# Performance work log

Hardware: AMD Instinct MI355X
Metric: run time of the kernel (lower is better)

Reference implementation:

```python
import jax, jax.numpy as jnp
import numpy as np

EPS = 1e-08


def setup_inputs() -> dict:
    key = jax.random.key(0)
    k1, k2, k3 = jax.random.split(key, 3)
    N, IN_DIM, OUT_DIM = 8192, 512, 512
    h = jax.random.normal(k1, (N, IN_DIM), dtype=jnp.float32)
    adj = jax.random.randint(k2, (N, N), 0, 2, dtype=jnp.int32)
    # nn.Linear(in_dim, out_dim, bias=False) weight: [out_dim, in_dim]
    W = jax.random.normal(k3, (OUT_DIM, IN_DIM), dtype=jnp.float32) * (1.0 / np.sqrt(IN_DIM))
    return {"h": h, "adj": adj, "W": W}


def reference(h, adj, W):
    # Wh = h @ W^T  -> [N, out_dim]
    Wh = h @ W.T
    N = Wh.shape[0]
    norms = jnp.linalg.norm(Wh, axis=1, keepdims=True)  # [N, 1]
    # cosine similarity [N, N]
    sim = (Wh @ Wh.T) / (norms * norms.T + EPS)
    mask = (adj > 0) | jnp.eye(N, dtype=bool)
    sim_masked = jnp.where(mask, sim, -jnp.inf)
    alpha = jax.nn.softmax(sim_masked, axis=1)
    return alpha @ Wh
```

## Files before the change

kernel.cpp:

```cpp
#include <hip/hip_runtime.h>
#include <hip/hip_bf16.h>
#include <stdint.h>

#define NN 8192
#define DD 512

typedef unsigned short u16;
typedef unsigned long long u64;
typedef __attribute__((ext_vector_type(8))) short short8;
typedef __attribute__((ext_vector_type(4))) float f32x4;

__device__ __forceinline__ void gld_lds16(const void* g, void* l) {
  __builtin_amdgcn_global_load_lds(
      (const __attribute__((address_space(1))) uint32_t*)(uintptr_t)g,
      (__attribute__((address_space(3))) uint32_t*)(uintptr_t)l,
      16, 0, 0);
}

__device__ __forceinline__ u16 f2bf(float f) {
  __hip_bfloat16 b = __float2bfloat16(f);
  return __builtin_bit_cast(u16, b);
}

__global__ void fill_kernel(float* __restrict__ p, int n, float v) {
  int i = blockIdx.x * 256 + threadIdx.x;
  int stride = gridDim.x * 256;
  for (; i < n; i += stride) p[i] = v;
}

__global__ void cvt4_kernel(const float4* __restrict__ src, ushort4* __restrict__ dst, int n4) {
  int i = blockIdx.x * 256 + threadIdx.x;
  int stride = gridDim.x * 256;
  for (; i < n4; i += stride) {
    float4 v = src[i];
    ushort4 o;
    o.x = f2bf(v.x); o.y = f2bf(v.y); o.z = f2bf(v.z); o.w = f2bf(v.w);
    dst[i] = o;
  }
}

__global__ void pack_adj_kernel(const int* __restrict__ adj, u16* __restrict__ mask) {
  const int row = blockIdx.x;
  const int t = threadIdx.x;
  const uint4* arow = (const uint4*)(adj + (size_t)row * NN);
  #pragma unroll
  for (int iter = 0; iter < 2; iter++) {
    const int c16 = iter * 256 + t;
    unsigned int bits = 0;
    #pragma unroll
    for (int g = 0; g < 4; g++) {
      uint4 v = arow[c16 * 4 + g];
      bits |= (v.x ? 1u : 0u) << (g * 4 + 0);
      bits |= (v.y ? 1u : 0u) << (g * 4 + 1);
      bits |= (v.z ? 1u : 0u) << (g * 4 + 2);
      bits |= (v.w ? 1u : 0u) << (g * 4 + 3);
    }
    mask[(size_t)row * (NN / 16) + c16] = (u16)bits;
  }
}

__global__ void rownorm_kernel(const float* __restrict__ Wh, float* __restrict__ invn) {
  int row = blockIdx.x;
  int l = threadIdx.x;
  const float4* p = (const float4*)(Wh + (size_t)row * DD);
  float4 a = p[l], b = p[l + 64];
  float s = a.x*a.x + a.y*a.y + a.z*a.z + a.w*a.w
          + b.x*b.x + b.y*b.y + b.z*b.z + b.w*b.w;
  #pragma unroll
  for (int off = 32; off; off >>= 1) s += __shfl_down(s, off);
  if (l == 0) invn[row] = 1.0f / sqrtf(s);
}

__global__ void u_wht_kernel(const float* __restrict__ Wh, const float* __restrict__ invn,
                             u16* __restrict__ U, u16* __restrict__ WhT) {
  __shared__ float tile[64][65];
  int i0 = blockIdx.x * 64, d0 = blockIdx.y * 64;
  int c = threadIdx.x & 63, rb = threadIdx.x >> 6;
  #pragma unroll
  for (int r = rb; r < 64; r += 4) {
    float v = Wh[(size_t)(i0 + r) * DD + d0 + c];
    tile[r][c] = v;
    U[(size_t)(i0 + r) * DD + d0 + c] = f2bf(v * invn[i0 + r]);
  }
  __syncthreads();
  #pragma unroll
  for (int r = rb; r < 64; r += 4) {
    WhT[(size_t)(d0 + r) * NN + i0 + c] = f2bf(tile[c][r]);
  }
}

__global__ void reduce_scale_kernel(float4* __restrict__ out, const float4* __restrict__ part1,
                                    const float* __restrict__ den) {
  int i4 = blockIdx.x * 256 + threadIdx.x;
  const int row = i4 >> 7;
  const float dinv = 1.0f / den[row];
  float4 a = out[i4], b = part1[i4];
  a.x = (a.x + b.x) * dinv;
  a.y = (a.y + b.y) * dinv;
  a.z = (a.z + b.z) * dinv;
  a.w = (a.w + b.w) * dinv;
  out[i4] = a;
}

template <int MODE>
__global__ void __launch_bounds__(256) gemm_bt(
    const u16* __restrict__ A, const u16* __restrict__ B,
    int Nn, int K, int kSplit,
    float* __restrict__ Cf0, float* __restrict__ Cf1,
    const u64* __restrict__ maskw, u16* __restrict__ Pb,
    float* __restrict__ den)
{
  __shared__ __align__(16) u16 As[128 * 32];
  __shared__ __align__(16) u16 Bs[128 * 32];

  const int tid = threadIdx.x;
  const int w = tid >> 6;
  const int lane = tid & 63;
  const int lm = lane & 15;
  const int q = lane >> 4;
  const int row0 = blockIdx.y * 128;
  const int col0 = blockIdx.x * 128;
  const int RM = (w >> 1) * 64;
  const int RN = (w & 1) * 64;

  const int sr = tid >> 2;
  const int sk = (tid & 3) * 8;

  int kBegin = 0, kEnd = K;
  if (MODE == 0) {
    kBegin = blockIdx.z ? kSplit : 0;
    kEnd   = blockIdx.z ? K : kSplit;
  }

  f32x4 acc[4][4];
  #pragma unroll
  for (int a_ = 0; a_ < 4; a_++)
    #pragma unroll
    for (int b_ = 0; b_ < 4; b_++)
      acc[a_][b_] = (f32x4){0.f, 0.f, 0.f, 0.f};

  const size_t Abase = (size_t)row0 * K;
  const size_t Bbase = (size_t)col0 * K;

  for (int k0 = kBegin; k0 < kEnd; k0 += 32) {
    __syncthreads();
    gld_lds16(A + Abase + (size_t)sr * K + k0 + sk,        (char*)As + w * 1024);
    gld_lds16(A + Abase + (size_t)(sr + 64) * K + k0 + sk, (char*)As + 4096 + w * 1024);
    gld_lds16(B + Bbase + (size_t)sr * K + k0 + sk,        (char*)Bs + w * 1024);
    gld_lds16(B + Bbase + (size_t)(sr + 64) * K + k0 + sk, (char*)Bs + 4096 + w * 1024);
    __syncthreads();

    short8 af[4], bfr[4];
    #pragma unroll
    for (int mt = 0; mt < 4; mt++)
      af[mt] = *(const short8*)&As[(RM + mt * 16 + lm) * 32 + q * 8];
    #pragma unroll
    for (int nt = 0; nt < 4; nt++)
      bfr[nt] = *(const short8*)&Bs[(RN + nt * 16 + lm) * 32 + q * 8];

    #pragma unroll
    for (int mt = 0; mt < 4; mt++)
      #pragma unroll
      for (int nt = 0; nt < 4; nt++)
        acc[mt][nt] = __builtin_amdgcn_mfma_f32_16x16x32_bf16(af[mt], bfr[nt], acc[mt][nt], 0, 0, 0);
  }

  float* const Cf = (MODE == 0 && blockIdx.z) ? Cf1 : Cf0;
  const int wordIdx = (col0 + RN) >> 6;
  #pragma unroll
  for (int mt = 0; mt < 4; mt++) {
    const int ib = row0 + RM + mt * 16 + q * 4;
    #pragma unroll
    for (int rr = 0; rr < 4; rr++) {
      const int i = ib + rr;
      if (MODE == 0) {
        #pragma unroll
        for (int nt = 0; nt < 4; nt++) {
          const int jc = col0 + RN + nt * 16 + lm;
          Cf[(size_t)i * Nn + jc] = acc[mt][nt][rr];
        }
      } else {
        const u64 wrd = maskw[(size_t)i * (NN / 64) + wordIdx];
        float psum = 0.f;
        #pragma unroll
        for (int nt = 0; nt < 4; nt++) {
          const int jc = col0 + RN + nt * 16 + lm;
          const bool on = ((wrd >> (nt * 16 + lm)) & 1ull) || (i == jc);
          const float p = on ? __expf(acc[mt][nt][rr]) : 0.0f;
          psum += p;
          Pb[(size_t)i * NN + jc] = f2bf(p);
        }
        #pragma unroll
        for (int off = 8; off; off >>= 1) psum += __shfl_down(psum, off, 16);
        if (lm == 0) atomicAdd(&den[i], psum);
      }
    }
  }
}

extern "C" void kernel_launch(void* const* d_in, const int* in_sizes, int n_in,
                              void* d_out, int out_size, void* d_ws, size_t ws_size,
                              hipStream_t stream) {
  const float* h = (const float*)d_in[0];
  const int* adj = (const int*)d_in[1];
  const float* W = (const float*)d_in[2];
  float* out = (float*)d_out;

  const size_t SZ_P    = (size_t)NN * NN * 2;
  const size_t SZ_MASK = (size_t)NN * NN / 8;
  const size_t SZ_WHT  = (size_t)DD * NN * 2;
  const size_t SZ_HB   = (size_t)NN * DD * 2;
  const size_t SZ_WB   = (size_t)DD * DD * 2;
  const size_t SZ_U    = (size_t)NN * DD * 2;
  const size_t SZ_WH   = (size_t)NN * DD * 4;
  const size_t NEEDED  = SZ_P + SZ_MASK + SZ_WHT + SZ_HB + SZ_WB + SZ_U + SZ_WH + 2 * (size_t)NN * 4;

  if (ws_size < NEEDED) {
    fill_kernel<<<256, 256, 0, stream>>>(out, out_size, 12345.0f);
    return;
  }

  char* ws = (char*)d_ws;
  size_t off = 0;
  u16*   P    = (u16*)(ws + off); off += SZ_P;
  u16*   mask = (u16*)(ws + off); off += SZ_MASK;
  u16*   WhT  = (u16*)(ws + off); off += SZ_WHT;
  u16*   hb   = (u16*)(ws + off); off += SZ_HB;
  u16*   Wb   = (u16*)(ws + off); off += SZ_WB;
  u16*   U    = (u16*)(ws + off); off += SZ_U;
  float* Wh   = (float*)(ws + off); off += SZ_WH;
  float* invn = (float*)(ws + off);
  float* den  = invn + NN;
  float* part1 = Wh;

  pack_adj_kernel<<<NN, 256, 0, stream>>>(adj, mask);
  fill_kernel<<<32, 256, 0, stream>>>(den, NN, 0.0f);
  cvt4_kernel<<<1024, 256, 0, stream>>>((const float4*)h, (ushort4*)hb, NN * DD / 4);
  cvt4_kernel<<<256, 256, 0, stream>>>((const float4*)W, (ushort4*)Wb, DD * DD / 4);
  gemm_bt<0><<<dim3(DD / 128, NN / 128, 1), 256, 0, stream>>>(
      hb, Wb, DD, DD, DD, Wh, nullptr, nullptr, nullptr, nullptr);
  rownorm_kernel<<<NN, 64, 0, stream>>>(Wh, invn);
  u_wht_kernel<<<dim3(NN / 64, DD / 64), 256, 0, stream>>>(Wh, invn, U, WhT);
  gemm_bt<1><<<dim3(NN / 128, NN / 128, 1), 256, 0, stream>>>(
      U, U, NN, DD, DD, nullptr, nullptr, (const u64*)mask, P, den);
  gemm_bt<0><<<dim3(DD / 128, NN / 128, 2), 256, 0, stream>>>(
      P, WhT, DD, NN, NN / 2, out, part1, nullptr, nullptr, nullptr);
  reduce_scale_kernel<<<NN * DD / 4 / 256, 256, 0, stream>>>(
      (float4*)out, (const float4*)part1, den);
}
```

Baseline: 707.3 us.

## Use full-width 128x512 tiles with 4-way split-K for P@Wh, bf16 partials

Replaces the second GEMM (P @ Wh) with a dedicated kernel whose 512-thread block computes a 128-row by full 512-column output tile. This lets each P tile be loaded once instead of four times across column blocks. K is split four ways, giving 256 blocks. Each split writes bf16 partials into reused workspace buffers, and a new reduce kernel sums them and applies the softmax denominator. The trade-offs are extra precision loss from bf16 partial storage, higher register pressure from 32 accumulators per thread, and a larger LDS footprint per block.

```diff
diff --git a/kernel.cpp b/kernel.cpp
--- a/kernel.cpp
+++ b/kernel.cpp
@@ -89,24 +89,11 @@
   }
 }
 
-__global__ void reduce_scale_kernel(float4* __restrict__ out, const float4* __restrict__ part1,
-                                    const float* __restrict__ den) {
-  int i4 = blockIdx.x * 256 + threadIdx.x;
-  const int row = i4 >> 7;
-  const float dinv = 1.0f / den[row];
-  float4 a = out[i4], b = part1[i4];
-  a.x = (a.x + b.x) * dinv;
-  a.y = (a.y + b.y) * dinv;
-  a.z = (a.z + b.z) * dinv;
-  a.w = (a.w + b.w) * dinv;
-  out[i4] = a;
-}
-
 template <int MODE>
 __global__ void __launch_bounds__(256) gemm_bt(
     const u16* __restrict__ A, const u16* __restrict__ B,
-    int Nn, int K, int kSplit,
-    float* __restrict__ Cf0, float* __restrict__ Cf1,
+    int Nn, int K,
+    float* __restrict__ Cf,
     const u64* __restrict__ maskw, u16* __restrict__ Pb,
     float* __restrict__ den)
 {
@@ -126,12 +113,6 @@
   const int sr = tid >> 2;
   const int sk = (tid & 3) * 8;
 
-  int kBegin = 0, kEnd = K;
-  if (MODE == 0) {
-    kBegin = blockIdx.z ? kSplit : 0;
-    kEnd   = blockIdx.z ? K : kSplit;
-  }
-
   f32x4 acc[4][4];
   #pragma unroll
   for (int a_ = 0; a_ < 4; a_++)
@@ -142,7 +123,7 @@
   const size_t Abase = (size_t)row0 * K;
   const size_t Bbase = (size_t)col0 * K;
 
-  for (int k0 = kBegin; k0 < kEnd; k0 += 32) {
+  for (int k0 = 0; k0 < K; k0 += 32) {
     __syncthreads();
     gld_lds16(A + Abase + (size_t)sr * K + k0 + sk,        (char*)As + w * 1024);
     gld_lds16(A + Abase + (size_t)(sr + 64) * K + k0 + sk, (char*)As + 4096 + w * 1024);
@@ -165,7 +146,6 @@
         acc[mt][nt] = __builtin_amdgcn_mfma_f32_16x16x32_bf16(af[mt], bfr[nt], acc[mt][nt], 0, 0, 0);
   }
 
-  float* const Cf = (MODE == 0 && blockIdx.z) ? Cf1 : Cf0;
   const int wordIdx = (col0 + RN) >> 6;
   #pragma unroll
   for (int mt = 0; mt < 4; mt++) {
@@ -198,6 +178,99 @@
   }
 }
 
+__global__ void __launch_bounds__(512, 2) gemm_out(
+    const u16* __restrict__ A,
+    const u16* __restrict__ B,
+    u16* const __restrict__* partv_unused,
+    u16* __restrict__ p0, u16* __restrict__ p1,
+    u16* __restrict__ p2, u16* __restrict__ p3)
+{
+  __shared__ __align__(16) u16 As[128 * 32];
+  __shared__ __align__(16) u16 Bs[512 * 32];
+
+  const int tid = threadIdx.x;
+  const int w = tid >> 6;
+  const int lane = tid & 63;
+  const int lm = lane & 15;
+  const int q = lane >> 4;
+  const int row0 = blockIdx.x * 128;
+  const int z = blockIdx.y;
+  const int RM = (w >> 2) * 64;
+  const int RN = (w & 3) * 128;
+
+  const int sr = tid >> 2;
+  const int sk = (tid & 3) * 8;
+
+  f32x4 acc[4][8];
+  #pragma unroll
+  for (int a_ = 0; a_ < 4; a_++)
+    #pragma unroll
+    for (int b_ = 0; b_ < 8; b_++)
+      acc[a_][b_] = (f32x4){0.f, 0.f, 0.f, 0.f};
+
+  const size_t Abase = (size_t)row0 * NN;
+  const int kBegin = z * (NN / 4), kEnd = (z + 1) * (NN / 4);
+
+  for (int k0 = kBegin; k0 < kEnd; k0 += 32) {
+    __syncthreads();
+    gld_lds16(A + Abase + (size_t)sr * NN + k0 + sk, (char*)As + w * 1024);
+    #pragma unroll
+    for (int c = 0; c < 4; c++)
+      gld_lds16(B + (size_t)(c * 128 + sr) * NN + k0 + sk, (char*)Bs + c * 8192 + w * 1024);
+    __syncthreads();
+
+    short8 af[4], bfr[8];
+    #pragma unroll
+    for (int mt = 0; mt < 4; mt++)
+      af[mt] = *(const short8*)&As[(RM + mt * 16 + lm) * 32 + q * 8];
+    #pragma unroll
+    for (int nt = 0; nt < 8; nt++)
+      bfr[nt] = *(const short8*)&Bs[(RN + nt * 16 + lm) * 32 + q * 8];
+
+    #pragma unroll
+    for (int mt = 0; mt < 4; mt++)
+      #pragma unroll
+      for (int nt = 0; nt < 8; nt++)
+        acc[mt][nt] = __builtin_amdgcn_mfma_f32_16x16x32_bf16(af[mt], bfr[nt], acc[mt][nt], 0, 0, 0);
+  }
+
+  u16* const part = (z == 0) ? p0 : (z == 1) ? p1 : (z == 2) ? p2 : p3;
+  #pragma unroll
+  for (int mt = 0; mt < 4; mt++) {
+    const int ib = row0 + RM + mt * 16 + q * 4;
+    #pragma unroll
+    for (int rr = 0; rr < 4; rr++) {
+      const int i = ib + rr;
+      #pragma unroll
+      for (int nt = 0; nt < 8; nt++) {
+        const int dc = RN + nt * 16 + lm;
+        part[(size_t)i * DD + dc] = f2bf(acc[mt][nt][rr]);
+      }
+    }
+  }
+}
+
+__global__ void reduce4_kernel(const uint4* __restrict__ p0, const uint4* __restrict__ p1,
+                               const uint4* __restrict__ p2, const uint4* __restrict__ p3,
+                               const float* __restrict__ den, float4* __restrict__ out) {
+  const int idx = blockIdx.x * 256 + threadIdx.x;
+  const int row = idx >> 6;
+  const float dinv = 1.0f / den[row];
+  float s[8] = {0, 0, 0, 0, 0, 0, 0, 0};
+  #pragma unroll
+  for (int zp = 0; zp < 4; zp++) {
+    const uint4 u = (zp == 0 ? p0 : zp == 1 ? p1 : zp == 2 ? p2 : p3)[idx];
+    s[0] += __uint_as_float(u.x << 16); s[1] += __uint_as_float(u.x & 0xffff0000u);
+    s[2] += __uint_as_float(u.y << 16); s[3] += __uint_as_float(u.y & 0xffff0000u);
+    s[4] += __uint_as_float(u.z << 16); s[5] += __uint_as_float(u.z & 0xffff0000u);
+    s[6] += __uint_as_float(u.w << 16); s[7] += __uint_as_float(u.w & 0xffff0000u);
+  }
+  float4 o0 = {s[0] * dinv, s[1] * dinv, s[2] * dinv, s[3] * dinv};
+  float4 o1 = {s[4] * dinv, s[5] * dinv, s[6] * dinv, s[7] * dinv};
+  out[idx * 2] = o0;
+  out[idx * 2 + 1] = o1;
+}
+
 extern "C" void kernel_launch(void* const* d_in, const int* in_sizes, int n_in,
                               void* d_out, int out_size, void* d_ws, size_t ws_size,
                               hipStream_t stream) {
@@ -231,20 +304,25 @@
   float* Wh   = (float*)(ws + off); off += SZ_WH;
   float* invn = (float*)(ws + off);
   float* den  = invn + NN;
-  float* part1 = Wh;
+
+  u16* part0 = U;
+  u16* part1 = hb;
+  u16* part2 = (u16*)Wh;
+  u16* part3 = (u16*)Wh + (size_t)NN * DD;
 
   pack_adj_kernel<<<NN, 256, 0, stream>>>(adj, mask);
   fill_kernel<<<32, 256, 0, stream>>>(den, NN, 0.0f);
   cvt4_kernel<<<1024, 256, 0, stream>>>((const float4*)h, (ushort4*)hb, NN * DD / 4);
   cvt4_kernel<<<256, 256, 0, stream>>>((const float4*)W, (ushort4*)Wb, DD * DD / 4);
-  gemm_bt<0><<<dim3(DD / 128, NN / 128, 1), 256, 0, stream>>>(
-      hb, Wb, DD, DD, DD, Wh, nullptr, nullptr, nullptr, nullptr);
+  gemm_bt<0><<<dim3(DD / 128, NN / 128), 256, 0, stream>>>(
+      hb, Wb, DD, DD, Wh, nullptr, nullptr, nullptr);
   rownorm_kernel<<<NN, 64, 0, stream>>>(Wh, invn);
   u_wht_kernel<<<dim3(NN / 64, DD / 64), 256, 0, stream>>>(Wh, invn, U, WhT);
-  gemm_bt<1><<<dim3(NN / 128, NN / 128, 1), 256, 0, stream>>>(
-      U, U, NN, DD, DD, nullptr, nullptr, (const u64*)mask, P, den);
-  gemm_bt<0><<<dim3(DD / 128, NN / 128, 2), 256, 0, stream>>>(
-      P, WhT, DD, NN, NN / 2, out, part1, nullptr, nullptr, nullptr);
-  reduce_scale_kernel<<<NN * DD / 4 / 256, 256, 0, stream>>>(
-      (float4*)out, (const float4*)part1, den);
-}
+  gemm_bt<1><<<dim3(NN / 128, NN / 128), 256, 0, stream>>>(
+      U, U, NN, DD, nullptr, (const u64*)mask, P, den);
+  gemm_out<<<dim3(NN / 128, 4), 512, 0, stream>>>(
+      P, WhT, nullptr, part0, part1, part2, part3);
+  reduce4_kernel<<<NN * DD / 8 / 256, 256, 0, stream>>>(
+      (const uint4*)part0, (const uint4*)part1, (const uint4*)part2, (const uint4*)part3,
+      den, (float4*)out);
+}
```

After: 670.9 us. 5.2% less time.
